# Kernel tuning notes

Measured on AMD Instinct MI355X. Metric: run time of the kernel, lower is better.

Reference implementation:

```python
import jax, jax.numpy as jnp
import numpy as np

B, CIN, H, W = 8, 128, 32, 32
COUT, K, STRIDE, PAD = 128, 3, 1, 1
DK, DV, NH = 64, 64, 8
DKH, DVH = DK // NH, DV // NH


def conv2d(x, w, b, stride, pad):
    out = jax.lax.conv_general_dilated(
        x, w, (stride, stride), [(pad, pad), (pad, pad)],
        dimension_numbers=("NCHW", "OIHW", "NCHW"))
    return out + b[None, :, None, None]


def rel_to_abs(x):
    # x: (b, Nh, L, 2L-1) relative -> (b, Nh, L, L) absolute via pad/reshape/slice
    b, nh, L, _ = x.shape
    x = jnp.pad(x, ((0, 0), (0, 0), (0, 0), (0, 1)))          # (b,Nh,L,2L)
    flat = x.reshape(b, nh, L * 2 * L)
    flat = jnp.pad(flat, ((0, 0), (0, 0), (0, L - 1)))
    final = flat.reshape(b, nh, L + 1, 2 * L - 1)
    return final[:, :, :L, L - 1:]


def relative_logits_1d(q, key_rel, Hh, Ww, Nh, case):
    # q: (b, Nh, x, y, dkh); key_rel: (2*len-1, dkh)
    rel = jnp.einsum("bhxyd,md->bhxym", q, key_rel)
    rel = rel.reshape(-1, Nh * Hh, Ww, 2 * Ww - 1)
    rel = rel_to_abs(rel)
    rel = rel.reshape(-1, Nh, Hh, Ww, Ww)
    rel = jnp.tile(rel[:, :, :, None, :, :], (1, 1, 1, Hh, 1, 1))  # (b,Nh,H,H,W,W)
    if case == "h":
        # torch .transpose(2,4).transpose(3,5)
        rel = rel.transpose(0, 1, 4, 5, 2, 3)
    return rel.reshape(-1, Nh, Hh * Ww, Hh * Ww)


def reference(x, w_general, b_general, w_qkv, b_qkv, w_out, b_out, key_rel_h, key_rel_w):
    batch, _, height, width = x.shape
    conv_out = conv2d(x, w_general, b_general, STRIDE, PAD)

    qkv = conv2d(x, w_qkv, b_qkv, 1, 0)
    q, k, v = jnp.split(qkv, [DK, 2 * DK], axis=1)
    # split heads: (B, Nh, c//Nh, H, W)
    q = q.reshape(batch, NH, DKH, height, width)
    k = k.reshape(batch, NH, DKH, height, width)
    v = v.reshape(batch, NH, DVH, height, width)
    # faithful to original bug: q / dkh**(-0.5) == q * sqrt(dkh)
    q = q / (DKH ** (-0.5))

    flat_q = q.reshape(batch, NH, height * width, DKH)
    flat_k = k.reshape(batch, NH, height * width, DKH)
    flat_v = v.reshape(batch, NH, height * width, DVH)

    logits = jnp.einsum("bhnd,bhmd->bhnm", flat_q, flat_k)

    # relative position logits
    q5 = q.transpose(0, 1, 3, 4, 2)  # (B, Nh, H, W, dkh)
    logits = logits + relative_logits_1d(q5, key_rel_h, height, width, NH, "h")
    logits = logits + relative_logits_1d(q5.transpose(0, 1, 3, 2, 4), key_rel_w, height, width, NH, "w")

    weights = jax.nn.softmax(logits, axis=-1)
    attn = jnp.einsum("bhnm,bhmd->bhnd", weights, flat_v)
    attn = attn.reshape(batch, NH, height, width, DVH)
    # combine heads: (B, Nh*dvh, H, W)
    attn = attn.transpose(0, 1, 4, 2, 3).reshape(batch, NH * DVH, height, width)
    attn = conv2d(attn, w_out, b_out, STRIDE, PAD)
    return jnp.concatenate((conv_out, attn), axis=1)


def setup_inputs():
    key = jax.random.key(0)
    ks = jax.random.split(key, 8)
    f = jnp.float32
    x = jax.random.normal(ks[0], (B, CIN, H, W), f)
    w_general = jax.random.normal(ks[1], (COUT - DV, CIN, K, K), f) * 0.02
    b_general = jnp.zeros((COUT - DV,), f)
    w_qkv = jax.random.normal(ks[2], (2 * DK + DV, CIN, 1, 1), f) * 0.05
    b_qkv = jnp.zeros((2 * DK + DV,), f)
    w_out = jax.random.normal(ks[3], (DV, DV, K, K), f) * 0.05
    b_out = jnp.zeros((DV,), f)
    key_rel_h = jax.random.normal(ks[4], (2 * H - 1, DKH), f)
    key_rel_w = jax.random.normal(ks[5], (2 * W - 1, DKH), f)
    return {"x": x, "w_general": w_general, "b_general": b_general,
            "w_qkv": w_qkv, "b_qkv": b_qkv, "w_out": w_out, "b_out": b_out,
            "key_rel_h": key_rel_h, "key_rel_w": key_rel_w}
```

## Files before the change

kernel.cpp:

```cpp
#include <hip/hip_runtime.h>
#include <hip/hip_bf16.h>


#define NP 1024
#define QSCALE 2.8284271247461903f
#define LOG2E  1.4426950408889634f

using bf16 = __hip_bfloat16;
typedef unsigned short ushort;
typedef unsigned int uint;
using bf16x8 = __attribute__((ext_vector_type(8))) short;
using f32x4  = __attribute__((ext_vector_type(4))) float;
using f32x2  = __attribute__((ext_vector_type(2))) float;

__device__ __forceinline__ float b2f(bf16 v) { return __bfloat162float(v); }
__device__ __forceinline__ ushort f2b(float v) {
  bf16 h = __float2bfloat16(v);
  ushort u; __builtin_memcpy(&u, &h, 2); return u;
}
__device__ __forceinline__ f32x2 up2(uint u) {
  f32x2 r;
  r[0] = __uint_as_float(u << 16);
  r[1] = __uint_as_float(u & 0xffff0000u);
  return r;
}

__device__ __forceinline__ float dot8(const float* a, const float* b) {
  float s = a[0] * b[0];
  s = fmaf(a[1], b[1], s); s = fmaf(a[2], b[2], s); s = fmaf(a[3], b[3], s);
  s = fmaf(a[4], b[4], s); s = fmaf(a[5], b[5], s); s = fmaf(a[6], b[6], s);
  s = fmaf(a[7], b[7], s);
  return s;
}

__device__ __forceinline__ int fenc(float f) { int i = __float_as_int(f); return i < 0 ? (i ^ 0x7fffffff) : i; }
__device__ __forceinline__ float fdec(int i) { return __int_as_float(i < 0 ? (i ^ 0x7fffffff) : i); }

#if defined(__has_builtin)
#if __has_builtin(__builtin_amdgcn_exp2f)
#define EXP2F __builtin_amdgcn_exp2f
#else
#define EXP2F exp2f
#endif
#else
#define EXP2F exp2f
#endif

#if defined(__has_builtin)
#if __has_builtin(__builtin_amdgcn_s_setprio)
#define SETPRIO(n) __builtin_amdgcn_s_setprio(n)
#else
#define SETPRIO(n) asm volatile("s_setprio " #n)
#endif
#else
#define SETPRIO(n) asm volatile("s_setprio " #n)
#endif

#define OFF_QBUF   0
#define OFF_KB16   524288
#define OFF_VTB    786432
#define OFF_XPB    1310720
#define OFF_APB    1902592
#define OFF_WGB    2198528
#define OFF_WOB    2235392
#define OFF_BG     2253824
#define OFF_BQKV   2253888
#define OFF_BO     2254080
#define OFF_KRH    2254144
#define OFF_KRW    2254648
#define OFF_FLAG   2255152
#define OFF_WQB    2255168

__global__ __launch_bounds__(256) void cvt_kernel(
    const void* __restrict__ p0, const void* __restrict__ p1, const void* __restrict__ p2,
    const void* __restrict__ p3, const void* __restrict__ p4, const void* __restrict__ p5,
    const void* __restrict__ p6, const void* __restrict__ p7, const void* __restrict__ p8,
    float* __restrict__ ws, int* __restrict__ flag)
{
  __shared__ int partial[4];
  __shared__ uint lds[64][65];
  int t = threadIdx.x;
  const unsigned* xraw = (const unsigned*)p0;
  int cnt = 0;
  for (int i = t; i < 1024; i += 256) {
    unsigned elo = (xraw[i] >> 7) & 0xffu;
    cnt += (elo >= 64u && elo <= 133u) ? 1 : 0;
  }
#pragma unroll
  for (int off = 1; off < 64; off <<= 1) cnt += __shfl_xor(cnt, off);
  if ((t & 63) == 0) partial[t >> 6] = cnt;
  __syncthreads();
  int tot = partial[0] + partial[1] + partial[2] + partial[3];
  int f32 = (tot >= 650) ? 0 : 1;
  if (blockIdx.x == 0 && t == 0) *flag = f32;

  int gsz = gridDim.x * 256;
  int gid = blockIdx.x * 256 + t;

  const void* src[5] = {p2, p4, p6, p7, p8};
  const int   n[5]    = {64, 192, 64, 504, 504};
  const int   doff[5] = {OFF_BG, OFF_BQKV, OFF_BO, OFF_KRH, OFF_KRW};
#pragma unroll
  for (int s = 0; s < 5; s++) {
    float* dst = ws + doff[s];
    if (f32) { const float* sp = (const float*)src[s];
      for (int i = gid; i < n[s]; i += gsz) dst[i] = sp[i];
    } else { const bf16* sp = (const bf16*)src[s];
      for (int i = gid; i < n[s]; i += gsz) dst[i] = b2f(sp[i]);
    }
  }

  {
    float4* z = (float4*)(ws + OFF_VTB);
    for (int i = gid; i < 131072; i += gsz) z[i] = float4{0.f, 0.f, 0.f, 0.f};
  }

  {
    uint4 z = {0u, 0u, 0u, 0u};
    uint4* xp = (uint4*)(ws + OFF_XPB);
    uint4* ap = (uint4*)(ws + OFF_APB);
    for (int s = gid; s < 9248; s += gsz) {
      int pb = s / 1156, rem = s - pb * 1156;
      int y = rem / 34, x = rem - y * 34;
      if (y == 0 || y == 33 || x == 0 || x == 33) {
        uint4* d1 = xp + (size_t)s * 16;
#pragma unroll
        for (int k = 0; k < 16; k++) d1[k] = z;
        uint4* d2 = ap + (size_t)s * 8;
#pragma unroll
        for (int k = 0; k < 8; k++) d2[k] = z;
      }
    }
  }

  {
    ushort* wgb = (ushort*)(ws + OFF_WGB);
    for (int s = gid; s < 73728; s += gsz) {
      int kykx = s >> 13, co = (s >> 7) & 63, ci = s & 127;
      int si = (co * 128 + ci) * 9 + kykx;
      wgb[s] = f32 ? f2b(((const float*)p1)[si]) : ((const ushort*)p1)[si];
    }
  }
  {
    ushort* wob = (ushort*)(ws + OFF_WOB);
    for (int s = gid; s < 36864; s += gsz) {
      int kykx = s >> 12, co = (s >> 6) & 63, ci = s & 63;
      int si = (co * 64 + ci) * 9 + kykx;
      wob[s] = f32 ? f2b(((const float*)p5)[si]) : ((const ushort*)p5)[si];
    }
  }
  {
    ushort* wqb = (ushort*)(ws + OFF_WQB);
    for (int s = gid; s < 24576; s += gsz) {
      wqb[s] = f32 ? f2b(((const float*)p3)[s]) : ((const ushort*)p3)[s];
    }
  }

  if (blockIdx.x < 128) {
    int w = t >> 6, lane = t & 63;
    int b = blockIdx.x >> 4;
    int pp0 = (blockIdx.x & 15) * 64;
    if (f32) {
      const float* xs = (const float*)p0 + (size_t)b * 131072 + pp0;
#pragma unroll 4
      for (int i = 0; i < 16; i++) {
        int cp = w * 16 + i;
        float v0 = xs[(size_t)(2 * cp) * 1024 + lane];
        float v1 = xs[(size_t)(2 * cp + 1) * 1024 + lane];
        lds[cp][lane] = (uint)f2b(v0) | ((uint)f2b(v1) << 16);
      }
    } else {
      const ushort* xs = (const ushort*)p0 + (size_t)b * 131072 + pp0;
#pragma unroll 4
      for (int i = 0; i < 16; i++) {
        int cp = w * 16 + i;
        uint v0 = xs[(size_t)(2 * cp) * 1024 + lane];
        uint v1 = xs[(size_t)(2 * cp + 1) * 1024 + lane];
        lds[cp][lane] = v0 | (v1 << 16);
      }
    }
    __syncthreads();
    uint* xp32 = (uint*)(ws + OFF_XPB);
#pragma unroll 4
    for (int i = 0; i < 16; i++) {
      int p = w * 16 + i;
      int pp = pp0 + p;
      int y = pp >> 5, x = pp & 31;
      xp32[((size_t)(b * 34 + y + 1) * 34 + x + 1) * 64 + lane] = lds[lane][p];
    }
  }
}

__global__ __launch_bounds__(256) void qkv_mfma_kernel(
    const ushort* __restrict__ xp, const ushort* __restrict__ wqb,
    const float* __restrict__ bias, float* __restrict__ qbuf,
    ushort* __restrict__ kb16, ushort* __restrict__ vtb)
{
  int pt = blockIdx.x;
  int b  = blockIdx.y;
  int lane = threadIdx.x & 63;
  int w = threadIdx.x >> 6;
  int n = lane & 15;
  int kg = lane >> 4;
  int p0 = pt * 16;
  int px = p0 + n;
  int y = px >> 5, x = px & 31;

  const ushort* bbase = xp + ((size_t)(b * 34 + y + 1) * 34 + (x + 1)) * 128 + kg * 8;
  bf16x8 Bf[4];
#pragma unroll
  for (int c = 0; c < 4; c++) Bf[c] = *(const bf16x8*)(bbase + c * 32);

  f32x4 acc0 = {0.f, 0.f, 0.f, 0.f};
  f32x4 acc1 = {0.f, 0.f, 0.f, 0.f};
  f32x4 acc2 = {0.f, 0.f, 0.f, 0.f};
  {
    const ushort* abase = wqb + (size_t)(w * 16 + n) * 128 + kg * 8;
#pragma unroll
    for (int c = 0; c < 4; c++) {
      bf16x8 A = *(const bf16x8*)(abase + c * 32);
      acc0 = __builtin_amdgcn_mfma_f32_16x16x32_bf16(A, Bf[c], acc0, 0, 0, 0);
    }
  }
  {
    const ushort* abase = wqb + (size_t)((w + 4) * 16 + n) * 128 + kg * 8;
#pragma unroll
    for (int c = 0; c < 4; c++) {
      bf16x8 A = *(const bf16x8*)(abase + c * 32);
      acc1 = __builtin_amdgcn_mfma_f32_16x16x32_bf16(A, Bf[c], acc1, 0, 0, 0);
    }
  }
  {
    const ushort* abase = wqb + (size_t)((w + 8) * 16 + n) * 128 + kg * 8;
#pragma unroll
    for (int c = 0; c < 4; c++) {
      bf16x8 A = *(const bf16x8*)(abase + c * 32);
      acc2 = __builtin_amdgcn_mfma_f32_16x16x32_bf16(A, Bf[c], acc2, 0, 0, 0);
    }
  }

#pragma unroll
  for (int r = 0; r < 4; r++) {
    int co = w * 16 + kg * 4 + r;
    float v = acc0[r] + bias[co];
    qbuf[((size_t)b * 64 + co) * NP + px] = v * QSCALE;
  }
#pragma unroll
  for (int r = 0; r < 4; r++) {
    int co = (w + 4) * 16 + kg * 4 + r;
    float v = acc1[r] + bias[co];
    kb16[((size_t)b * 64 + (co - 64)) * NP + px] = f2b(v);
  }
#pragma unroll
  for (int r = 0; r < 4; r++) {
    int co = (w + 8) * 16 + kg * 4 + r;
    float v = acc2[r] + bias[co];
    int ch = co - 128;
    int h = ch >> 3;
    int d0 = px & 7;
    int m  = (ch & 7) * 128 + (px >> 3);
    vtb[((size_t)(b * 8 + h) * 16 + d0) * 1024 + m] = f2b(v);
  }
}

template <int CINT>
__device__ __forceinline__ void conv_body(
    const ushort* __restrict__ xp, const ushort* __restrict__ wp,
    const float* __restrict__ bias, void* __restrict__ out,
    int co_base, const int* __restrict__ flag, int pt, int b)
{
  int lane = threadIdx.x & 63;
  int w = threadIdx.x >> 6;
  int n = lane & 15;
  int kg = lane >> 4;
  int p0 = pt * 16;
  int y = p0 >> 5, x0 = p0 & 31;

  const ushort* abase = wp + (size_t)(w * 16 + n) * CINT + kg * 8;
  const ushort* bbase = xp + ((size_t)(b * 34 + y) * 34 + x0 + n) * CINT + kg * 8;

  f32x4 acc0 = {0.f, 0.f, 0.f, 0.f};
  f32x4 acc1 = {0.f, 0.f, 0.f, 0.f};
#pragma unroll
  for (int c = 0; c < CINT / 32; c++) {
    int ci0 = c * 32;
#pragma unroll
    for (int kp = 0; kp < 9; kp++) {
      int ky = kp / 3, kx = kp - ky * 3;
      bf16x8 A = *(const bf16x8*)(abase + (size_t)kp * 64 * CINT + ci0);
      bf16x8 B = *(const bf16x8*)(bbase + (size_t)(ky * 34 + kx) * CINT + ci0);
      if (kp & 1) acc1 = __builtin_amdgcn_mfma_f32_16x16x32_bf16(A, B, acc1, 0, 0, 0);
      else        acc0 = __builtin_amdgcn_mfma_f32_16x16x32_bf16(A, B, acc0, 0, 0, 0);
    }
  }

  int f32o = *flag;
#pragma unroll
  for (int r = 0; r < 4; r++) {
    int co = w * 16 + kg * 4 + r;
    float v = acc0[r] + acc1[r] + bias[co];
    size_t eoff = ((size_t)b * 128 + co_base + co) * 1024 + p0 + n;
    if (f32o) ((float*)out)[eoff] = v;
    else ((bf16*)out)[eoff] = __float2bfloat16(v);
  }
}

__global__ __launch_bounds__(256, 4) void attn_conv_kernel(
    const float* __restrict__ qbuf, const ushort* __restrict__ kb16, const ushort* __restrict__ vtb,
    const float* __restrict__ krh, const float* __restrict__ krw,
    ushort* __restrict__ apb,
    const ushort* __restrict__ xp, const ushort* __restrict__ wgb,
    const float* __restrict__ bg, void* __restrict__ out, const int* __restrict__ flag)
{
  int bx = blockIdx.x;
  if (bx >= 1024) {
    int id = bx - 1024;
    conv_body<128>(xp, wgb, bg, out, 0, flag, id & 63, id >> 6);
    return;
  }
  SETPRIO(1);

  __shared__ float bw2[2][NP];
  __shared__ float bhT[2][32][32];
  __shared__ __align__(16) float krhs[64][8];
  __shared__ __align__(16) float krws[64][8];
  __shared__ __align__(16) char uni[10240];
  __shared__ float lred[4][16];
  __shared__ int smax[3];
  float (*qsT)[32][8]        = (float (*)[32][8])uni;
  ushort (*Plds)[4][16][40]  = (ushort (*)[4][16][40])uni;

  int t = threadIdx.x;
  int cp = bx & 15, h = (bx >> 4) & 7, b = bx >> 7;
  int C0 = cp * 2;
  const float* qbase = qbuf + ((size_t)b * 64 + h * 8) * NP;
  const uint4* kb4 = (const uint4*)(kb16 + ((size_t)b * 64 + h * 8) * NP);
  const ushort* vth = vtb + (size_t)(b * 8 + h) * 16384;

  if (t < 3) smax[t] = (t == 0) ? 0 : fenc(-3.0e38f);

  for (int idx = t; idx < 63 * 8; idx += 256) {
    krhs[idx >> 3][idx & 7] = krh[idx];
    krws[idx >> 3][idx & 7] = krw[idx];
  }
  for (int idx = t; idx < 512; idx += 256) {
    int cs = idx >> 8, d = (idx >> 5) & 7, r = idx & 31;
    qsT[cs][r][d] = qbase[(size_t)d * NP + r * 32 + (C0 + cs)];
  }
  float kn2 = 0.f;
#pragma unroll
  for (int rr = 0; rr < 4; rr++) {
    uint4 ku = kb4[rr * 256 + t];
    f32x2 k0 = up2(ku.x), k1 = up2(ku.y), k2 = up2(ku.z), k3 = up2(ku.w);
    f32x2 s2 = k0 * k0;
    s2 = __builtin_elementwise_fma(k1, k1, s2);
    s2 = __builtin_elementwise_fma(k2, k2, s2);
    s2 = __builtin_elementwise_fma(k3, k3, s2);
    kn2 = fmaxf(kn2, s2[0] + s2[1]);
  }
  __syncthreads();
  atomicMax(&smax[0], __float_as_int(kn2));

  float bwm = -3.0e38f;
  for (int idx = t; idx < 2048; idx += 256) {
    int cs = idx >> 10, m = idx & 1023;
    int rg = m >> 5, j2 = m & 31;
    float s = dot8(qsT[cs][rg], krws[j2 - rg + 31]) * LOG2E;
    bw2[cs][m] = s;
    bwm = fmaxf(bwm, s);
  }
  float bhm = -3.0e38f;
  for (int idx = t; idx < 2048; idx += 256) {
    int cs = idx >> 10, r = idx & 1023;
    int i = r >> 5, J = r & 31;
    float s = dot8(qsT[cs][i], krhs[J - (C0 + cs) + 31]) * LOG2E;
    bhT[cs][i][J] = s;
    bhm = fmaxf(bhm, s);
  }
  atomicMax(&smax[1], fenc(bwm));
  atomicMax(&smax[2], fenc(bhm));
  __syncthreads();

  float kmaxn = sqrtf(__int_as_float(smax[0]));
  float bmax = fdec(smax[1]) + fdec(smax[2]);

  int w = t >> 6, lane = t & 63;
  int quad = lane >> 4, nIdx = lane & 15;
  int n0 = cp * 64 + w * 16;
  int nQ = n0 + nIdx;
  int Cs = w >> 1;
  int J = ((w & 1) << 4) + nIdx;

  const bf16x8 zero8 = {0, 0, 0, 0, 0, 0, 0, 0};

  const float* qrow = qbase + (size_t)nQ * 8;
  bf16x8 Bq = zero8;
  float nn = 0.f;
  ushort ub[8];
#pragma unroll
  for (int d = 0; d < 8; d++) {
    float v = qrow[d] * LOG2E;
    ub[d] = f2b(v);
    float vr = __uint_as_float((uint)ub[d] << 16);
    nn = fmaf(vr, vr, nn);
  }
  if (quad == 0) {
#pragma unroll
    for (int d = 0; d < 8; d++) Bq[d] = (short)ub[d];
  }
  float Mn = sqrtf(nn) * kmaxn + bmax;

  f32x4 accE = {0.f, 0.f, 0.f, 0.f};
  f32x4 accD = {0.f, 0.f, 0.f, 0.f};
  float lpE = 0.f, lpD = 0.f;

#pragma unroll 2
  for (int mc = 0; mc < 32; ++mc) {
    int mb = mc * 32;
    ushort* prow = &Plds[mc & 1][w][nIdx][0];
    float pre = bhT[Cs][mc][J] - Mn;
    bf16x8 Ak0 = *(const bf16x8*)(kb4 + mb + nIdx);
    bf16x8 Ak1 = *(const bf16x8*)(kb4 + mb + 16 + nIdx);
    if (quad != 0) { Ak0 = zero8; Ak1 = zero8; }
    f32x4 S0 = __builtin_amdgcn_mfma_f32_16x16x32_bf16(Ak0, Bq, f32x4{0.f,0.f,0.f,0.f}, 0, 0, 0);
    f32x4 S1 = __builtin_amdgcn_mfma_f32_16x16x32_bf16(Ak1, Bq, f32x4{0.f,0.f,0.f,0.f}, 0, 0, 0);
    float4 bwA = *(const float4*)&bw2[Cs][mb + (quad << 2)];
    float4 bwB = *(const float4*)&bw2[Cs][mb + 16 + (quad << 2)];
    float p0 = EXP2F(S0[0] + bwA.x + pre);
    float p1 = EXP2F(S0[1] + bwA.y + pre);
    float p2 = EXP2F(S0[2] + bwA.z + pre);
    float p3 = EXP2F(S0[3] + bwA.w + pre);
    float p4 = EXP2F(S1[0] + bwB.x + pre);
    float p5 = EXP2F(S1[1] + bwB.y + pre);
    float p6 = EXP2F(S1[2] + bwB.z + pre);
    float p7 = EXP2F(S1[3] + bwB.w + pre);
    float ps = ((p0 + p1) + (p2 + p3)) + ((p4 + p5) + (p6 + p7));
    uint2 w0, w1;
    w0.x = (uint)f2b(p0) | ((uint)f2b(p1) << 16);
    w0.y = (uint)f2b(p2) | ((uint)f2b(p3) << 16);
    w1.x = (uint)f2b(p4) | ((uint)f2b(p5) << 16);
    w1.y = (uint)f2b(p6) | ((uint)f2b(p7) << 16);
    *(uint2*)(prow + (quad << 2))        = w0;
    *(uint2*)(prow + 16 + (quad << 2))   = w1;
    bf16x8 Ap = *(const bf16x8*)(prow + (quad << 3));
    bf16x8 Bv = *(const bf16x8*)(vth + (size_t)nIdx * 1024 + mb + (quad << 3));
    if (mc & 1) { accD = __builtin_amdgcn_mfma_f32_16x16x32_bf16(Ap, Bv, accD, 0, 0, 0); lpD += ps; }
    else        { accE = __builtin_amdgcn_mfma_f32_16x16x32_bf16(Ap, Bv, accE, 0, 0, 0); lpE += ps; }
  }

  f32x4 accO = accE + accD;
  float lpart = lpE + lpD;

  lpart += __shfl_xor(lpart, 16);
  lpart += __shfl_xor(lpart, 32);
  if (lane < 16) lred[w][lane] = lpart;
  float4 lr4 = *(const float4*)&lred[w][quad << 2];
  const float lr[4] = {lr4.x, lr4.y, lr4.z, lr4.w};

  SETPRIO(0);
  if (nIdx < 8) {
#pragma unroll
    for (int r = 0; r < 4; ++r) {
      int n = n0 + (quad << 2) + r;
      float v = accO[r] / lr[r];
      apb[((size_t)(b * 34 + (n >> 5) + 1) * 34 + (n & 31) + 1) * 64 + h * 8 + nIdx] = f2b(v);
    }
  }
}

template <int CINT>
__global__ __launch_bounds__(256) void conv_mfma_kernel(
    const ushort* __restrict__ xp, const ushort* __restrict__ wp,
    const float* __restrict__ bias, void* __restrict__ out,
    int co_base, const int* __restrict__ flag)
{
  conv_body<CINT>(xp, wp, bias, out, co_base, flag, blockIdx.x, blockIdx.y);
}

extern "C" void kernel_launch(void* const* d_in, const int* in_sizes, int n_in,
                              void* d_out, int out_size, void* d_ws, size_t ws_size,
                              hipStream_t stream) {
  float* ws = (float*)d_ws;
  float*  qbuf  = ws + OFF_QBUF;
  ushort* kb16  = (ushort*)(ws + OFF_KB16);
  ushort* vtb   = (ushort*)(ws + OFF_VTB);
  ushort* xpb   = (ushort*)(ws + OFF_XPB);
  ushort* apb   = (ushort*)(ws + OFF_APB);
  ushort* wgb   = (ushort*)(ws + OFF_WGB);
  ushort* wob   = (ushort*)(ws + OFF_WOB);
  ushort* wqb   = (ushort*)(ws + OFF_WQB);
  float*  bgf   = ws + OFF_BG;
  float*  bqkvf = ws + OFF_BQKV;
  float*  bof   = ws + OFF_BO;
  float*  krhf  = ws + OFF_KRH;
  float*  krwf  = ws + OFF_KRW;
  int*    flag  = (int*)(ws + OFF_FLAG);

  cvt_kernel<<<512, 256, 0, stream>>>(d_in[0], d_in[1], d_in[2], d_in[3], d_in[4],
                                      d_in[5], d_in[6], d_in[7], d_in[8], ws, flag);
  qkv_mfma_kernel<<<dim3(64, 8), 256, 0, stream>>>(xpb, wqb, bqkvf, qbuf, kb16, vtb);
  attn_conv_kernel<<<1536, 256, 0, stream>>>(qbuf, kb16, vtb, krhf, krwf, apb,
                                             xpb, wgb, bgf, d_out, flag);
  conv_mfma_kernel<64><<<dim3(64, 8), 256, 0, stream>>>(apb, wob, bof, d_out, 64, flag);
}
```

Baseline: 142.8 us.

## Split attention key loop across two wave groups with 512-thread blocks

Doubles the attention block size to 512 threads so two groups of four waves each take alternating key chunks of the softmax-times-V loop. Partial accumulators and row sums are then combined through shared memory before normalisation and the store. The intent is more waves in flight to hide MFMA, exp and memory latency on each query tile. In exchange it adds two block barriers and an LDS reduction, leaves half the threads idle in the fused conv blocks, and the tighter launch bounds may cause register pressure or spills.

New measurement: 157.1 us. +10.0%, slower.

```diff
diff --git a/kernel.cpp b/kernel.cpp
--- a/kernel.cpp
+++ b/kernel.cpp
@@ -305,7 +305,7 @@
   }
 }
 
-__global__ __launch_bounds__(256, 4) void attn_conv_kernel(
+__global__ __launch_bounds__(512, 8) void attn_conv_kernel(
     const float* __restrict__ qbuf, const ushort* __restrict__ kb16, const ushort* __restrict__ vtb,
     const float* __restrict__ krh, const float* __restrict__ krw,
     ushort* __restrict__ apb,
@@ -315,7 +315,7 @@
   int bx = blockIdx.x;
   if (bx >= 1024) {
     int id = bx - 1024;
-    conv_body<128>(xp, wgb, bg, out, 0, flag, id & 63, id >> 6);
+    if (threadIdx.x < 256) conv_body<128>(xp, wgb, bg, out, 0, flag, id & 63, id >> 6);
     return;
   }
   SETPRIO(1);
@@ -327,8 +327,9 @@
   __shared__ __align__(16) char uni[10240];
   __shared__ float lred[4][16];
   __shared__ int smax[3];
-  float (*qsT)[32][8]        = (float (*)[32][8])uni;
-  ushort (*Plds)[4][16][40]  = (ushort (*)[4][16][40])uni;
+  float (*qsT)[32][8]       = (float (*)[32][8])uni;
+  ushort (*Plds)[16][40]    = (ushort (*)[16][40])uni;
+  float (*scr)[8]           = (float (*)[8])uni;
 
   int t = threadIdx.x;
   int cp = bx & 15, h = (bx >> 4) & 7, b = bx >> 7;
@@ -339,18 +340,21 @@
 
   if (t < 3) smax[t] = (t == 0) ? 0 : fenc(-3.0e38f);
 
-  for (int idx = t; idx < 63 * 8; idx += 256) {
+  for (int idx = t; idx < 63 * 8; idx += 512) {
     krhs[idx >> 3][idx & 7] = krh[idx];
     krws[idx >> 3][idx & 7] = krw[idx];
   }
-  for (int idx = t; idx < 512; idx += 256) {
-    int cs = idx >> 8, d = (idx >> 5) & 7, r = idx & 31;
-    qsT[cs][r][d] = qbase[(size_t)d * NP + r * 32 + (C0 + cs)];
+  if (t < 512) {
+    int idx = t;
+    if (idx < 512) {
+      int cs = idx >> 8, d = (idx >> 5) & 7, r = idx & 31;
+      qsT[cs][r][d] = qbase[(size_t)d * NP + r * 32 + (C0 + cs)];
+    }
   }
   float kn2 = 0.f;
 #pragma unroll
-  for (int rr = 0; rr < 4; rr++) {
-    uint4 ku = kb4[rr * 256 + t];
+  for (int rr = 0; rr < 2; rr++) {
+    uint4 ku = kb4[rr * 512 + t];
     f32x2 k0 = up2(ku.x), k1 = up2(ku.y), k2 = up2(ku.z), k3 = up2(ku.w);
     f32x2 s2 = k0 * k0;
     s2 = __builtin_elementwise_fma(k1, k1, s2);
@@ -362,7 +366,7 @@
   atomicMax(&smax[0], __float_as_int(kn2));
 
   float bwm = -3.0e38f;
-  for (int idx = t; idx < 2048; idx += 256) {
+  for (int idx = t; idx < 2048; idx += 512) {
     int cs = idx >> 10, m = idx & 1023;
     int rg = m >> 5, j2 = m & 31;
     float s = dot8(qsT[cs][rg], krws[j2 - rg + 31]) * LOG2E;
@@ -370,7 +374,7 @@
     bwm = fmaxf(bwm, s);
   }
   float bhm = -3.0e38f;
-  for (int idx = t; idx < 2048; idx += 256) {
+  for (int idx = t; idx < 2048; idx += 512) {
     int cs = idx >> 10, r = idx & 1023;
     int i = r >> 5, J = r & 31;
     float s = dot8(qsT[cs][i], krhs[J - (C0 + cs) + 31]) * LOG2E;
@@ -385,11 +389,13 @@
   float bmax = fdec(smax[1]) + fdec(smax[2]);
 
   int w = t >> 6, lane = t & 63;
+  int w3 = w & 3;
+  int par = w >> 2;
   int quad = lane >> 4, nIdx = lane & 15;
-  int n0 = cp * 64 + w * 16;
+  int n0 = cp * 64 + w3 * 16;
   int nQ = n0 + nIdx;
-  int Cs = w >> 1;
-  int J = ((w & 1) << 4) + nIdx;
+  int Cs = w3 >> 1;
+  int J = ((w3 & 1) << 4) + nIdx;
 
   const bf16x8 zero8 = {0, 0, 0, 0, 0, 0, 0, 0};
 
@@ -413,11 +419,11 @@
   f32x4 accE = {0.f, 0.f, 0.f, 0.f};
   f32x4 accD = {0.f, 0.f, 0.f, 0.f};
   float lpE = 0.f, lpD = 0.f;
+  ushort* prow = &Plds[w][nIdx][0];
 
 #pragma unroll 2
-  for (int mc = 0; mc < 32; ++mc) {
+  for (int mc = par; mc < 32; mc += 2) {
     int mb = mc * 32;
-    ushort* prow = &Plds[mc & 1][w][nIdx][0];
     float pre = bhT[Cs][mc][J] - Mn;
     bf16x8 Ak0 = *(const bf16x8*)(kb4 + mb + nIdx);
     bf16x8 Ak1 = *(const bf16x8*)(kb4 + mb + 16 + nIdx);
@@ -444,28 +450,41 @@
     *(uint2*)(prow + 16 + (quad << 2))   = w1;
     bf16x8 Ap = *(const bf16x8*)(prow + (quad << 3));
     bf16x8 Bv = *(const bf16x8*)(vth + (size_t)nIdx * 1024 + mb + (quad << 3));
-    if (mc & 1) { accD = __builtin_amdgcn_mfma_f32_16x16x32_bf16(Ap, Bv, accD, 0, 0, 0); lpD += ps; }
+    if (mc & 2) { accD = __builtin_amdgcn_mfma_f32_16x16x32_bf16(Ap, Bv, accD, 0, 0, 0); lpD += ps; }
     else        { accE = __builtin_amdgcn_mfma_f32_16x16x32_bf16(Ap, Bv, accE, 0, 0, 0); lpE += ps; }
   }
 
   f32x4 accO = accE + accD;
   float lpart = lpE + lpD;
 
-  lpart += __shfl_xor(lpart, 16);
-  lpart += __shfl_xor(lpart, 32);
-  if (lane < 16) lred[w][lane] = lpart;
-  float4 lr4 = *(const float4*)&lred[w][quad << 2];
-  const float lr[4] = {lr4.x, lr4.y, lr4.z, lr4.w};
-
+  __syncthreads();
+  if (par) {
+    float* s5 = scr[w3 * 64 + lane];
+    s5[0] = accO[0]; s5[1] = accO[1]; s5[2] = accO[2]; s5[3] = accO[3];
+    s5[4] = lpart;
+  }
+  __syncthreads();
+  if (par == 0) {
+    const float* s5 = scr[w3 * 64 + lane];
+    accO[0] += s5[0]; accO[1] += s5[1]; accO[2] += s5[2]; accO[3] += s5[3];
+    lpart += s5[4];
+
+    lpart += __shfl_xor(lpart, 16);
+    lpart += __shfl_xor(lpart, 32);
+    if (lane < 16) lred[w3][lane] = lpart;
+    float4 lr4 = *(const float4*)&lred[w3][quad << 2];
+    const float lr[4] = {lr4.x, lr4.y, lr4.z, lr4.w};
+
+    if (nIdx < 8) {
+#pragma unroll
+      for (int r = 0; r < 4; ++r) {
+        int n = n0 + (quad << 2) + r;
+        float v = accO[r] / lr[r];
+        apb[((size_t)(b * 34 + (n >> 5) + 1) * 34 + (n & 31) + 1) * 64 + h * 8 + nIdx] = f2b(v);
+      }
+    }
+  }
   SETPRIO(0);
-  if (nIdx < 8) {
-#pragma unroll
-    for (int r = 0; r < 4; ++r) {
-      int n = n0 + (quad << 2) + r;
-      float v = accO[r] / lr[r];
-      apb[((size_t)(b * 34 + (n >> 5) + 1) * 34 + (n & 31) + 1) * 64 + h * 8 + nIdx] = f2b(v);
-    }
-  }
 }
 
 template <int CINT>
@@ -499,7 +518,7 @@
   cvt_kernel<<<512, 256, 0, stream>>>(d_in[0], d_in[1], d_in[2], d_in[3], d_in[4],
                                       d_in[5], d_in[6], d_in[7], d_in[8], ws, flag);
   qkv_mfma_kernel<<<dim3(64, 8), 256, 0, stream>>>(xpb, wqb, bqkvf, qbuf, kb16, vtb);
-  attn_conv_kernel<<<1536, 256, 0, stream>>>(qbuf, kb16, vtb, krhf, krwf, apb,
+  attn_conv_kernel<<<1536, 512, 0, stream>>>(qbuf, kb16, vtb, krhf, krwf, apb,
                                              xpb, wgb, bgf, d_out, flag);
   conv_mfma_kernel<64><<<dim3(64, 8), 256, 0, stream>>>(apb, wob, bof, d_out, 64, flag);
 }
```
